# Performance work log

Hardware: AMD Instinct MI355X
Metric: run time of the kernel (lower is better)

Reference implementation:

```python
import jax, jax.numpy as jnp
import numpy as np
from jax import lax

G, NPER, K = 64, 1024, 512          # graphs, nodes per graph, kept per graph (ceil(0.5*1024))
N, E = G * NPER, 1_048_576          # total nodes, total edges
F, H, C = 128, 128, 10              # in_feats, hidden_dim, num_classes


def gcn(x, src, dst, ew, W, b, num_nodes):
    """PyG GCNConv: D^{-1/2}(A+I)D^{-1/2} X W + b, with edge weights ew."""
    xw = x @ W                                              # [N, H]
    deg = jax.ops.segment_sum(ew, dst, num_segments=num_nodes) + 1.0  # +1 self loop
    dinv = lax.rsqrt(deg)
    coef = dinv[src] * dinv[dst] * ew                       # [E]
    agg = jax.ops.segment_sum(coef[:, None] * xw[src], dst, num_segments=num_nodes)
    return agg + (dinv * dinv)[:, None] * xw + b            # self-loop term + bias


def setup_inputs() -> dict:
    key = jax.random.key(0)
    ks = jax.random.split(key, 10)
    x = jax.random.normal(ks[0], (N, F), jnp.float32)
    # intra-graph random edges: dst forced into same graph block as src
    src = jax.random.randint(ks[1], (E,), 0, N, dtype=jnp.int32)
    dst = (src // NPER) * NPER + jax.random.randint(ks[2], (E,), 0, NPER, dtype=jnp.int32)
    edge_index = jnp.stack([src, dst])                      # [2, E]
    batch = jnp.repeat(jnp.arange(G, dtype=jnp.int32), NPER)
    W1 = jax.random.normal(ks[3], (F, H), jnp.float32) / np.sqrt(F)
    b1 = jnp.zeros((H,), jnp.float32)
    p = jax.random.normal(ks[4], (H,), jnp.float32) / np.sqrt(H)   # TopKPooling score vector
    W2 = jax.random.normal(ks[5], (H, H), jnp.float32) / np.sqrt(H)
    b2 = jnp.zeros((H,), jnp.float32)
    Wl = jax.random.normal(ks[6], (H, C), jnp.float32) / np.sqrt(H)
    bl = jnp.zeros((C,), jnp.float32)
    return dict(x=x, edge_index=edge_index, batch=batch, W1=W1, b1=b1, p=p, W2=W2, b2=b2, Wl=Wl, bl=bl)


def reference(x, edge_index, batch, W1, b1, p, W2, b2, Wl, bl):
    src, dst = edge_index[0], edge_index[1]
    ew1 = jnp.ones((E,), x.dtype)
    h = jax.nn.relu(gcn(x, src, dst, ew1, W1, b1, N))       # conv1 + relu

    # --- TopKPooling: score = tanh(x.p/||p||), keep top-K per graph, gate x by score ---
    score = jnp.tanh((h @ p) / jnp.linalg.norm(p))          # [N]
    vals, idx = lax.top_k(score.reshape(G, NPER), K)        # per-graph top-k, [G, K]
    perm = (idx + jnp.arange(G, dtype=idx.dtype)[:, None] * NPER).reshape(-1)  # global ids [G*K]
    h2 = h[perm] * vals.reshape(-1, 1)                      # gated kept nodes [G*K, H]

    # edge re-index: keep only edges with both endpoints surviving (mask via weight 0)
    new_id = jnp.full((N,), -1, jnp.int32).at[perm].set(jnp.arange(G * K, dtype=jnp.int32))
    s2, d2 = new_id[src], new_id[dst]
    mask = (s2 >= 0) & (d2 >= 0)
    ew2 = mask.astype(h.dtype)
    s2 = jnp.where(mask, s2, 0)
    d2 = jnp.where(mask, d2, 0)

    h3 = jax.nn.relu(gcn(h2, s2, d2, ew2, W2, b2, G * K))   # conv2 + relu

    pooled = h3.reshape(G, K, H).mean(axis=1)               # global_mean_pool (equal counts)
    return pooled @ Wl + bl                                 # [G, C]
```

## Files before the change

kernel.cpp:

```cpp
#include <hip/hip_runtime.h>

#define NNODES 65536
#define NEDGES 1048576
#define NGRAPH 64
#define NPERG  1024
#define KEEP   512
#define M2     (NGRAPH * KEEP)
#define HD     128
#define NC     10
#define EMAX   20480

#define OW1 0
#define OW2 16384
#define OWL 32768
#define OB1 34048
#define OB2 34176
#define OP  34304
#define OBL 34432
#define NCVT 34448

typedef __attribute__((ext_vector_type(8))) short bf16x8;
typedef __attribute__((ext_vector_type(4))) float f32x4;

__device__ __forceinline__ float bf2f(unsigned short u) {
    return __uint_as_float(((unsigned int)u) << 16);
}
__device__ __forceinline__ unsigned short f2bf(float f) {
    unsigned int u = __float_as_uint(f);
    unsigned int r = (u + 0x7FFFu + ((u >> 16) & 1u)) >> 16;
    return (unsigned short)r;
}

__global__ __launch_bounds__(256) void prep_kernel(
    const void* __restrict__ W1, const void* __restrict__ b1, const void* __restrict__ p,
    const void* __restrict__ W2, const void* __restrict__ b2, const void* __restrict__ Wl,
    const void* __restrict__ bl, int* __restrict__ flag, float* __restrict__ cw,
    float* __restrict__ invnorm, int* __restrict__ new_id, int* __restrict__ ghist,
    int* __restrict__ gcur0, float* __restrict__ pooled,
    unsigned short* __restrict__ w1t, unsigned short* __restrict__ w2t) {
    int bid = blockIdx.x, t = threadIdx.x;
    const unsigned short* w1u = (const unsigned short*)W1;
    int local = 0;
    for (int i = t; i < 512; i += 256) {
        unsigned short u = w1u[2 * i];
        int e = (u >> 7) & 0xFF;
        local += (e >= 100 && e <= 140) ? 1 : 0;
    }
    __shared__ int red[256];
    red[t] = local;
    __syncthreads();
    for (int off = 128; off; off >>= 1) {
        if (t < off) red[t] += red[t + off];
        __syncthreads();
    }
    int fl = (red[0] >= 384) ? 1 : 0;
    if (bid == 0 && t == 0) flag[0] = fl;

    if (bid < 135) {
        int gid = bid * 256 + t;
        if (gid < NCVT) {
            const void* srcp; int idx;
            if (gid < OB1) {
                if (gid < OW2)      { srcp = W1; idx = gid - OW1; }
                else if (gid < OWL) { srcp = W2; idx = gid - OW2; }
                else                { srcp = Wl; idx = gid - OWL; }
            } else {
                if (gid < OB2)      { srcp = b1; idx = gid - OB1; }
                else if (gid < OP)  { srcp = b2; idx = gid - OB2; }
                else if (gid < OBL) { srcp = p;  idx = gid - OP; }
                else                { srcp = bl; idx = gid - OBL; }
            }
            float v;
            if (gid >= OWL && gid < OB1 && idx >= 1280) v = 0.f;
            else if (gid >= OBL && idx >= NC) v = 0.f;
            else if (fl) v = bf2f(((const unsigned short*)srcp)[idx]);
            else v = ((const float*)srcp)[idx];
            cw[gid] = v;
            if (gid < OW2) {
                int k = gid >> 7, n = gid & 127;
                w1t[n * 128 + k] = f2bf(v);
            } else if (gid < OWL) {
                int r = gid - OW2;
                int k = r >> 7, n = r & 127;
                w2t[n * 128 + k] = f2bf(v);
            }
        }
    } else if (bid == 135) {
        __shared__ float s2a[128];
        float pv = 0.f;
        if (t < 128) pv = fl ? bf2f(((const unsigned short*)p)[t]) : ((const float*)p)[t];
        if (t < 128) s2a[t] = pv * pv;
        __syncthreads();
        for (int off = 64; off; off >>= 1) {
            if (t < off) s2a[t] += s2a[t + off];
            __syncthreads();
        }
        if (t == 0) invnorm[0] = 1.0f / sqrtf(s2a[0]);
    } else {
        int i = (bid - 136) * 256 + t;
        new_id[i] = -1;
        if (i < NGRAPH) { ghist[i] = 0; gcur0[i] = 0; }
        if (i < NGRAPH * HD) pooled[i] = 0.f;
    }
}

__global__ __launch_bounds__(256) void hist_kernel(const int* __restrict__ src,
                                                   int* __restrict__ ghist) {
    __shared__ int lh[NGRAPH];
    int tid = threadIdx.x;
    if (tid < NGRAPH) lh[tid] = 0;
    __syncthreads();
    int e0 = blockIdx.x * 4096;
    for (int k = 0; k < 16; k++) atomicAdd(&lh[src[e0 + k * 256 + tid] >> 10], 1);
    __syncthreads();
    if (tid < NGRAPH) atomicAdd(&ghist[tid], lh[tid]);
}
__global__ __launch_bounds__(256) void binpass_kernel(const int* __restrict__ src,
                                                      const int* __restrict__ dst,
                                                      const int* __restrict__ ghist,
                                                      int* __restrict__ gcur0,
                                                      unsigned int* __restrict__ elist) {
    __shared__ int gh[NGRAPH];
    __shared__ int gbS[NGRAPH];
    __shared__ int lh[NGRAPH];
    __shared__ int lbase[NGRAPH];
    int tid = threadIdx.x;
    if (tid < NGRAPH) { gh[tid] = ghist[tid]; lh[tid] = 0; }
    __syncthreads();
    if (tid == 0) {
        int s = 0;
        for (int i = 0; i < NGRAPH; i++) { gbS[i] = s; s += gh[i]; }
    }
    __syncthreads();
    int e0 = blockIdx.x * 4096;
    int gs[16]; unsigned int pk[16];
    for (int k = 0; k < 16; k++) {
        int e = e0 + k * 256 + tid;
        int s = src[e], d = dst[e];
        gs[k] = s >> 10;
        pk[k] = (unsigned)(s & 1023) | ((unsigned)(d & 1023) << 10);
        atomicAdd(&lh[gs[k]], 1);
    }
    __syncthreads();
    if (tid < NGRAPH) { lbase[tid] = gbS[tid] + atomicAdd(&gcur0[tid], lh[tid]); lh[tid] = 0; }
    __syncthreads();
    for (int k = 0; k < 16; k++) {
        int g = gs[k];
        int pos = lbase[g] + atomicAdd(&lh[g], 1);
        elist[pos] = pk[k];
    }
}

__global__ __launch_bounds__(1024) void g1csr_kernel(
    const unsigned int* __restrict__ elist, const int* __restrict__ ghist,
    unsigned short* __restrict__ csr16, int* __restrict__ node_base,
    int* __restrict__ deg_out, float* __restrict__ dinv_out,
    const void* __restrict__ Araw, const unsigned short* __restrict__ Wtb,
    unsigned int* __restrict__ Cb, const int* __restrict__ flag) {
    __shared__ unsigned short sc[EMAX];
    __shared__ int cnt[NPERG];
    __shared__ int cur[NPERG];
    __shared__ int wsum[16];
    __shared__ int gh[NGRAPH];
    __shared__ int baseS, nS;
    int bid = blockIdx.x, t = threadIdx.x;
    if (bid < NGRAPH) {
        int g = bid;
        cnt[t] = 0;
        if (t < NGRAPH) gh[t] = ghist[t];
        __syncthreads();
        if (t == 0) {
            int s = 0;
            for (int i = 0; i < g; i++) s += gh[i];
            baseS = s; nS = gh[g];
        }
        __syncthreads();
        int base = baseS;
        int n = nS; if (n > EMAX) n = EMAX;
        for (int j = t; j < n; j += 1024) atomicAdd(&cnt[(elist[base + j] >> 10) & 1023], 1);
        __syncthreads();
        int v = cnt[t];
        int lane = t & 63;
        int x = v;
        for (int off = 1; off < 64; off <<= 1) {
            int y = __shfl_up(x, off);
            if (lane >= off) x += y;
        }
        if (lane == 63) wsum[t >> 6] = x;
        __syncthreads();
        if (t < 16) {
            int wv = wsum[t];
            int wx = wv;
            for (int off = 1; off < 16; off <<= 1) {
                int y = __shfl_up(wx, off);
                if (t >= off) wx += y;
            }
            wsum[t] = wx - wv;
        }
        __syncthreads();
        int excl = x - v + wsum[t >> 6];
        cur[t] = excl;
        deg_out[g * NPERG + t] = v;
        dinv_out[g * NPERG + t] = rsqrtf((float)v + 1.0f);
        node_base[g * NPERG + t] = base + excl;
        __syncthreads();
        for (int j = t; j < n; j += 1024) {
            unsigned int pk = elist[base + j];
            int d = (pk >> 10) & 1023;
            int pos = atomicAdd(&cur[d], 1);
            sc[pos] = (unsigned short)(pk & 1023);
        }
        __syncthreads();
        for (int j = t; j < n; j += 1024) csr16[base + j] = sc[j];
        return;
    }
    int row0 = (bid - NGRAPH) * 256;
    int wave = t >> 6, lane = t & 63;
    int r0 = row0 + wave * 16;
    int row = r0 + (lane & 15);
    int ko = (lane >> 4) * 8;
    f32x4 acc[8];
#pragma unroll
    for (int c = 0; c < 8; c++) acc[c] = (f32x4){0.f, 0.f, 0.f, 0.f};
    bf16x8 afr[4];
    if (flag[0]) {
        const unsigned short* arow = (const unsigned short*)Araw + (size_t)row * HD + ko;
#pragma unroll
        for (int kk = 0; kk < 4; kk++) afr[kk] = *(const bf16x8*)(arow + kk * 32);
    } else {
        const float* arow = (const float*)Araw + (size_t)row * HD + ko;
#pragma unroll
        for (int kk = 0; kk < 4; kk++) {
            float4 f0 = *(const float4*)(arow + kk * 32);
            float4 f1 = *(const float4*)(arow + kk * 32 + 4);
            bf16x8 a;
            a[0] = (short)f2bf(f0.x); a[1] = (short)f2bf(f0.y);
            a[2] = (short)f2bf(f0.z); a[3] = (short)f2bf(f0.w);
            a[4] = (short)f2bf(f1.x); a[5] = (short)f2bf(f1.y);
            a[6] = (short)f2bf(f1.z); a[7] = (short)f2bf(f1.w);
            afr[kk] = a;
        }
    }
    const unsigned short* brow = Wtb + (lane & 15) * HD + ko;
#pragma unroll
    for (int kk = 0; kk < 4; kk++) {
#pragma unroll
        for (int c = 0; c < 8; c++) {
            bf16x8 b = *(const bf16x8*)(brow + c * 16 * HD + kk * 32);
            acc[c] = __builtin_amdgcn_mfma_f32_16x16x32_bf16(afr[kk], b, acc[c], 0, 0, 0);
        }
    }
    int orow0 = r0 + (lane >> 4) * 4;
    bool even = !(lane & 1);
#pragma unroll
    for (int c = 0; c < 8; c++) {
#pragma unroll
        for (int j = 0; j < 4; j++) {
            float v = acc[c][j];
            float pt = __shfl_xor(v, 1);
            if (even) {
                unsigned int u = (unsigned int)f2bf(v) | ((unsigned int)f2bf(pt) << 16);
                Cb[(size_t)(orow0 + j) * 64 + ((c * 16 + (lane & 15)) >> 1)] = u;
            }
        }
    }
}

__global__ __launch_bounds__(256) void s1_pull(const unsigned short* __restrict__ csr16,
                                               const int* __restrict__ node_base,
                                               const int* __restrict__ deg,
                                               const float* __restrict__ dinv,
                                               const unsigned int* __restrict__ xwb,
                                               const float* __restrict__ b1,
                                               const float* __restrict__ pvec,
                                               const float* __restrict__ invnorm,
                                               float* __restrict__ h,
                                               float* __restrict__ score) {
    int b = blockIdx.x;
    int xcd = b & 7, j = b >> 3;
    int g = (j >> 8) * 8 + xcd;
    int n = g * NPERG + (j & 255) * 4 + (threadIdx.x >> 6);
    int lane = threadIdx.x & 63;
    int gb = g * NPERG;
    int base = node_base[n], cnt = deg[n];
    int e = 0; float ds = 0.f;
    if (lane < cnt) {
        e = csr16[base + lane];
        ds = dinv[gb + e];
    }
    float a0 = 0.f, a1 = 0.f;
    int klim = cnt < 64 ? cnt : 64;
    int k = 0;
    for (; k + 3 < klim; k += 4) {
        int s0 = __shfl(e, k), s1 = __shfl(e, k + 1);
        int s2 = __shfl(e, k + 2), s3 = __shfl(e, k + 3);
        float d0 = __shfl(ds, k), d1 = __shfl(ds, k + 1);
        float d2 = __shfl(ds, k + 2), d3 = __shfl(ds, k + 3);
        unsigned int u0 = xwb[(size_t)(gb + s0) * 64 + lane];
        unsigned int u1 = xwb[(size_t)(gb + s1) * 64 + lane];
        unsigned int u2 = xwb[(size_t)(gb + s2) * 64 + lane];
        unsigned int u3 = xwb[(size_t)(gb + s3) * 64 + lane];
        a0 += d0 * __uint_as_float(u0 << 16); a1 += d0 * __uint_as_float(u0 & 0xFFFF0000u);
        a0 += d1 * __uint_as_float(u1 << 16); a1 += d1 * __uint_as_float(u1 & 0xFFFF0000u);
        a0 += d2 * __uint_as_float(u2 << 16); a1 += d2 * __uint_as_float(u2 & 0xFFFF0000u);
        a0 += d3 * __uint_as_float(u3 << 16); a1 += d3 * __uint_as_float(u3 & 0xFFFF0000u);
    }
    for (; k < klim; k++) {
        int sk = __shfl(e, k);
        float dk = __shfl(ds, k);
        unsigned int u = xwb[(size_t)(gb + sk) * 64 + lane];
        a0 += dk * __uint_as_float(u << 16); a1 += dk * __uint_as_float(u & 0xFFFF0000u);
    }
    for (; k < cnt; k++) {
        int sk = csr16[base + k];
        float dk = dinv[gb + sk];
        unsigned int u = xwb[(size_t)(gb + sk) * 64 + lane];
        a0 += dk * __uint_as_float(u << 16); a1 += dk * __uint_as_float(u & 0xFFFF0000u);
    }
    float dn = dinv[n];
    float self = dn * dn;
    unsigned int us = xwb[(size_t)n * 64 + lane];
    float2 bb = ((const float2*)b1)[lane];
    float h0 = fmaxf(dn * a0 + self * __uint_as_float(us << 16) + bb.x, 0.f);
    float h1 = fmaxf(dn * a1 + self * __uint_as_float(us & 0xFFFF0000u) + bb.y, 0.f);
    float2 ho = {h0, h1};
    ((float2*)h)[(size_t)n * 64 + lane] = ho;
    float2 pp = ((const float2*)pvec)[lane];
    float sv = h0 * pp.x + h1 * pp.y;
    for (int off = 32; off; off >>= 1) sv += __shfl_down(sv, off);
    if (lane == 0) score[n] = tanhf(sv * invnorm[0]);
}

__global__ __launch_bounds__(1024) void topk_kernel(const float* __restrict__ score,
                                                    float* __restrict__ vals,
                                                    int* __restrict__ perm,
                                                    int* __restrict__ new_id) {
    __shared__ float sv[1024];
    __shared__ int si[1024];
    int g = blockIdx.x, t = threadIdx.x;
    sv[t] = score[g * NPERG + t];
    si[t] = t;
    __syncthreads();
    for (int k = 2; k <= 1024; k <<= 1) {
        for (int j = k >> 1; j > 0; j >>= 1) {
            int l = t ^ j;
            if (l > t) {
                bool desc = ((t & k) == 0);
                float va = sv[t], vb = sv[l];
                int ia = si[t], ib = si[l];
                bool gab = (va > vb) || (va == vb && ia < ib);
                if (gab != desc) { sv[t] = vb; si[t] = ib; sv[l] = va; si[l] = ia; }
            }
            __syncthreads();
        }
    }
    if (t < KEEP) {
        int node = g * NPERG + si[t];
        int slot = g * KEEP + t;
        vals[slot] = sv[t];
        perm[slot] = node;
        new_id[node] = slot;
    }
}

__global__ __launch_bounds__(512) void g2deg_kernel(
    const unsigned int* __restrict__ elist, const int* __restrict__ ghist,
    const int* __restrict__ new_id, float* __restrict__ dinv2,
    const float* __restrict__ h, const int* __restrict__ perm,
    const float* __restrict__ vals, const unsigned short* __restrict__ Wtb,
    float* __restrict__ C) {
    __shared__ int d2[KEEP];
    __shared__ int gh[NGRAPH];
    __shared__ int baseS, nS;
    int bid = blockIdx.x, t = threadIdx.x;
    if (bid < NGRAPH) {
        int g = bid;
        if (t < KEEP) d2[t] = 0;
        if (t < NGRAPH) gh[t] = ghist[t];
        __syncthreads();
        if (t == 0) {
            int s = 0;
            for (int i = 0; i < g; i++) s += gh[i];
            baseS = s; nS = gh[g];
        }
        __syncthreads();
        int base = baseS, n = nS;
        int gb = g * NPERG;
        int kb = g * KEEP;
        for (int j = t; j < n; j += 512) {
            unsigned int pk = elist[base + j];
            int s = pk & 1023, d = (pk >> 10) & 1023;
            int ns = new_id[gb + s], nd = new_id[gb + d];
            if (ns >= 0 && nd >= 0) atomicAdd(&d2[nd - kb], 1);
        }
        __syncthreads();
        if (t < KEEP) dinv2[kb + t] = rsqrtf((float)d2[t] + 1.0f);
        return;
    }
    int row0 = (bid - NGRAPH) * 128;
    int wave = t >> 6, lane = t & 63;
    int r0 = row0 + wave * 16;
    int m = r0 + (lane & 15);
    int ko = (lane >> 4) * 8;
    float sc = vals[m];
    const float* arow = h + (size_t)perm[m] * HD + ko;
    bf16x8 afr[4];
#pragma unroll
    for (int kk = 0; kk < 4; kk++) {
        float4 f0 = *(const float4*)(arow + kk * 32);
        float4 f1 = *(const float4*)(arow + kk * 32 + 4);
        bf16x8 a;
        a[0] = (short)f2bf(f0.x * sc); a[1] = (short)f2bf(f0.y * sc);
        a[2] = (short)f2bf(f0.z * sc); a[3] = (short)f2bf(f0.w * sc);
        a[4] = (short)f2bf(f1.x * sc); a[5] = (short)f2bf(f1.y * sc);
        a[6] = (short)f2bf(f1.z * sc); a[7] = (short)f2bf(f1.w * sc);
        afr[kk] = a;
    }
    f32x4 acc[8];
#pragma unroll
    for (int c = 0; c < 8; c++) acc[c] = (f32x4){0.f, 0.f, 0.f, 0.f};
    const unsigned short* brow = Wtb + (lane & 15) * HD + ko;
#pragma unroll
    for (int kk = 0; kk < 4; kk++) {
#pragma unroll
        for (int c = 0; c < 8; c++) {
            bf16x8 b = *(const bf16x8*)(brow + c * 16 * HD + kk * 32);
            acc[c] = __builtin_amdgcn_mfma_f32_16x16x32_bf16(afr[kk], b, acc[c], 0, 0, 0);
        }
    }
    int orow0 = r0 + (lane >> 4) * 4;
    bool even = !(lane & 1);
    float2* C2 = (float2*)C;
#pragma unroll
    for (int c = 0; c < 8; c++) {
#pragma unroll
        for (int j = 0; j < 4; j++) {
            float v = acc[c][j];
            float pt = __shfl_xor(v, 1);
            if (even) {
                float2 o = {v, pt};
                C2[(size_t)(orow0 + j) * 64 + ((c * 16 + (lane & 15)) >> 1)] = o;
            }
        }
    }
}

__global__ __launch_bounds__(256) void s2_pull(const unsigned short* __restrict__ csr16,
                                               const int* __restrict__ node_base,
                                               const int* __restrict__ deg,
                                               const int* __restrict__ perm,
                                               const int* __restrict__ new_id,
                                               const float* __restrict__ dinv2,
                                               const float* __restrict__ xw2,
                                               const float* __restrict__ b2,
                                               float* __restrict__ pooled) {
    __shared__ float pr[HD];
    __shared__ int cnk[4][64];
    __shared__ float cds[4][64];
    int tid = threadIdx.x;
    if (tid < HD) pr[tid] = 0.f;
    __syncthreads();
    int b = blockIdx.x;
    int xcd = b & 7, j = b >> 3;
    int g = (j >> 7) * 8 + xcd;
    int wv = tid >> 6;
    int m = g * KEEP + (j & 127) * 4 + wv;
    int lane = tid & 63;
    int node = perm[m];
    int gb = node & ~(NPERG - 1);
    int base = node_base[node], cnt = deg[node];
    int nk = 0; float ds = 0.f;
    if (lane < cnt) {
        int ns = new_id[gb + csr16[base + lane]];
        if (ns >= 0) { nk = ns; ds = dinv2[ns]; }
    }
    unsigned long long msk = __ballot(ds != 0.f);
    int pos = __popcll(msk & ((1ull << lane) - 1ull));
    if (ds != 0.f) { cnk[wv][pos] = nk; cds[wv][pos] = ds; }
    int na = __popcll(msk);
    const float2* xf2 = (const float2*)xw2;
    float a0 = 0.f, a1 = 0.f;
    int k = 0;
    for (; k + 3 < na; k += 4) {
        int s0 = cnk[wv][k], s1 = cnk[wv][k + 1];
        int s2 = cnk[wv][k + 2], s3 = cnk[wv][k + 3];
        float d0 = cds[wv][k], d1 = cds[wv][k + 1];
        float d2 = cds[wv][k + 2], d3 = cds[wv][k + 3];
        float2 v0 = xf2[(size_t)s0 * 64 + lane];
        float2 v1 = xf2[(size_t)s1 * 64 + lane];
        float2 v2 = xf2[(size_t)s2 * 64 + lane];
        float2 v3 = xf2[(size_t)s3 * 64 + lane];
        a0 += d0 * v0.x; a1 += d0 * v0.y;
        a0 += d1 * v1.x; a1 += d1 * v1.y;
        a0 += d2 * v2.x; a1 += d2 * v2.y;
        a0 += d3 * v3.x; a1 += d3 * v3.y;
    }
    for (; k < na; k++) {
        int sk = cnk[wv][k];
        float dk = cds[wv][k];
        float2 v = xf2[(size_t)sk * 64 + lane];
        a0 += dk * v.x; a1 += dk * v.y;
    }
    for (int kk = 64; kk < cnt; kk++) {
        int ns = new_id[gb + csr16[base + kk]];
        if (ns >= 0) {
            float dk = dinv2[ns];
            float2 v = xf2[(size_t)ns * 64 + lane];
            a0 += dk * v.x; a1 += dk * v.y;
        }
    }
    float dn = dinv2[m];
    float self = dn * dn;
    float2 xs = xf2[(size_t)m * 64 + lane];
    float2 bb = ((const float2*)b2)[lane];
    float o0 = fmaxf(dn * a0 + self * xs.x + bb.x, 0.f);
    float o1 = fmaxf(dn * a1 + self * xs.y + bb.y, 0.f);
    atomicAdd(&pr[lane * 2], o0);
    atomicAdd(&pr[lane * 2 + 1], o1);
    __syncthreads();
    if (tid < HD) atomicAdd(&pooled[g * HD + tid], pr[tid]);
}

__global__ __launch_bounds__(128) void outk_kernel(const float* __restrict__ pooled,
                                                   const float* __restrict__ Wl,
                                                   const float* __restrict__ bl,
                                                   void* __restrict__ outv,
                                                   const int* __restrict__ flag) {
    int g = blockIdx.x, t = threadIdx.x;
    __shared__ float sp[HD];
    sp[t] = pooled[g * HD + t] * (1.0f / KEEP);
    __syncthreads();
    if (t < NC) {
        float acc = bl[t];
        for (int hh = 0; hh < HD; hh++) acc += sp[hh] * Wl[hh * NC + t];
        if (flag[0]) ((unsigned short*)outv)[g * NC + t] = f2bf(acc);
        else         ((float*)outv)[g * NC + t] = acc;
    }
}

extern "C" void kernel_launch(void* const* d_in, const int* in_sizes, int n_in,
                              void* d_out, int out_size, void* d_ws, size_t ws_size,
                              hipStream_t stream) {
    const int* ei   = (const int*)d_in[1];
    const int* srcv = ei;
    const int* dstv = ei + NEDGES;

    char* w = (char*)d_ws;
    const size_t MB = 1u << 20;
    const size_t KB = 1024;
    float* dinv1     = (float*)(w + 0);
    float* score     = (float*)(w + 256 * KB);
    float* vals      = (float*)(w + 512 * KB);
    int*   perm      = (int*)(w + 640 * KB);
    int*   new_id    = (int*)(w + 768 * KB);
    int*   deg1      = (int*)(w + 1024 * KB);
    int*   node_base = (int*)(w + 1280 * KB);
    float* dinv2     = (float*)(w + 1536 * KB);
    float* invnorm   = (float*)(w + 1664 * KB);
    int*   flag      = (int*)(w + 1664 * KB + 64);
    int*   ghist     = (int*)(w + 1664 * KB + 1024);
    int*   gcur0     = (int*)(w + 1664 * KB + 2048);
    float* cw        = (float*)(w + 1700 * KB);
    float* pooled    = (float*)(w + 1840 * KB);
    unsigned short* w1t = (unsigned short*)(w + 1880 * KB);
    unsigned short* w2t = (unsigned short*)(w + 1912 * KB);
    unsigned int* xw1b = (unsigned int*)(w + 2 * MB);
    float* xw2  = (float*)(w + 18 * MB);
    float* agg  = (float*)(w + 34 * MB);
    unsigned int* elist    = (unsigned int*)(w + 66 * MB);
    unsigned short* csr16  = (unsigned short*)(w + 70 * MB);

    float* W1f = cw + OW1; float* W2f = cw + OW2; float* Wlf = cw + OWL;
    float* b1f = cw + OB1; float* b2f = cw + OB2; float* pf  = cw + OP;
    float* blf = cw + OBL;
    (void)W1f; (void)W2f;

    prep_kernel<<<392, 256, 0, stream>>>(d_in[3], d_in[4], d_in[5], d_in[6], d_in[7],
                                         d_in[8], d_in[9], flag, cw, invnorm, new_id,
                                         ghist, gcur0, pooled, w1t, w2t);
    hist_kernel<<<256, 256, 0, stream>>>(srcv, ghist);
    binpass_kernel<<<256, 256, 0, stream>>>(srcv, dstv, ghist, gcur0, elist);
    g1csr_kernel<<<NGRAPH + NNODES / 256, 1024, 0, stream>>>(
        elist, ghist, csr16, node_base, deg1, dinv1, d_in[0], w1t, xw1b, flag);
    s1_pull<<<NNODES / 4, 256, 0, stream>>>(csr16, node_base, deg1, dinv1, xw1b, b1f, pf,
                                            invnorm, agg, score);
    topk_kernel<<<NGRAPH, 1024, 0, stream>>>(score, vals, perm, new_id);
    g2deg_kernel<<<NGRAPH + M2 / 128, 512, 0, stream>>>(
        elist, ghist, new_id, dinv2, agg, perm, vals, w2t, xw2);
    s2_pull<<<M2 / 4, 256, 0, stream>>>(csr16, node_base, deg1, perm, new_id, dinv2,
                                        xw2, b2f, pooled);
    outk_kernel<<<NGRAPH, 128, 0, stream>>>(pooled, Wlf, blf, d_out, flag);

    (void)in_sizes; (void)n_in; (void)out_size; (void)ws_size;
}
```

Before: 264.7 us.

## Fuse edge histogram into prep, store conv1 output as bf16, unroll gather by eight

Moves the per-graph source-edge histogram into extra blocks of the prep kernel, which now write per-block partial histograms. The binning kernel reduces those partials itself, so one launch and the global atomics are gone. The conv1 output h is stored as packed bf16 instead of fp32, halving the write in s1_pull and the gathered read in g2deg. The s1_pull neighbour gather gains an 8-wide unrolled loop to keep more loads in flight. The cost is an extra rounding of h before the gating multiply, and every binpass block redundantly re-reducing 256×64 partials.

```diff
diff --git a/kernel.cpp b/kernel.cpp
--- a/kernel.cpp
+++ b/kernel.cpp
@@ -37,7 +37,8 @@
     const void* __restrict__ bl, int* __restrict__ flag, float* __restrict__ cw,
     float* __restrict__ invnorm, int* __restrict__ new_id, int* __restrict__ ghist,
     int* __restrict__ gcur0, float* __restrict__ pooled,
-    unsigned short* __restrict__ w1t, unsigned short* __restrict__ w2t) {
+    unsigned short* __restrict__ w1t, unsigned short* __restrict__ w2t,
+    const int* __restrict__ src, int* __restrict__ phist) {
     int bid = blockIdx.x, t = threadIdx.x;
     const unsigned short* w1u = (const unsigned short*)W1;
     int local = 0;
@@ -47,6 +48,7 @@
         local += (e >= 100 && e <= 140) ? 1 : 0;
     }
     __shared__ int red[256];
+    __shared__ int lh[NGRAPH];
     red[t] = local;
     __syncthreads();
     for (int off = 128; off; off >>= 1) {
@@ -96,36 +98,45 @@
             __syncthreads();
         }
         if (t == 0) invnorm[0] = 1.0f / sqrtf(s2a[0]);
-    } else {
+    } else if (bid < 392) {
         int i = (bid - 136) * 256 + t;
         new_id[i] = -1;
         if (i < NGRAPH) { ghist[i] = 0; gcur0[i] = 0; }
         if (i < NGRAPH * HD) pooled[i] = 0.f;
-    }
-}
-
-__global__ __launch_bounds__(256) void hist_kernel(const int* __restrict__ src,
-                                                   int* __restrict__ ghist) {
-    __shared__ int lh[NGRAPH];
-    int tid = threadIdx.x;
-    if (tid < NGRAPH) lh[tid] = 0;
-    __syncthreads();
-    int e0 = blockIdx.x * 4096;
-    for (int k = 0; k < 16; k++) atomicAdd(&lh[src[e0 + k * 256 + tid] >> 10], 1);
-    __syncthreads();
-    if (tid < NGRAPH) atomicAdd(&ghist[tid], lh[tid]);
-}
+    } else {
+        if (t < NGRAPH) lh[t] = 0;
+        __syncthreads();
+        int e0 = (bid - 392) * 4096;
+        for (int k = 0; k < 16; k++) atomicAdd(&lh[src[e0 + k * 256 + t] >> 10], 1);
+        __syncthreads();
+        if (t < NGRAPH) phist[(bid - 392) * 64 + t] = lh[t];
+    }
+}
+
 __global__ __launch_bounds__(256) void binpass_kernel(const int* __restrict__ src,
                                                       const int* __restrict__ dst,
-                                                      const int* __restrict__ ghist,
+                                                      const int* __restrict__ phist,
+                                                      int* __restrict__ ghist,
                                                       int* __restrict__ gcur0,
                                                       unsigned int* __restrict__ elist) {
     __shared__ int gh[NGRAPH];
     __shared__ int gbS[NGRAPH];
     __shared__ int lh[NGRAPH];
     __shared__ int lbase[NGRAPH];
+    __shared__ int qsum[4][NGRAPH];
     int tid = threadIdx.x;
-    if (tid < NGRAPH) { gh[tid] = ghist[tid]; lh[tid] = 0; }
+    {
+        int g = tid & 63, q = tid >> 6;
+        int s = 0;
+        for (int b = q * 64; b < q * 64 + 64; b++) s += phist[b * 64 + g];
+        qsum[q][g] = s;
+    }
+    __syncthreads();
+    if (tid < NGRAPH) {
+        gh[tid] = qsum[0][tid] + qsum[1][tid] + qsum[2][tid] + qsum[3][tid];
+        lh[tid] = 0;
+        if (blockIdx.x == 0) ghist[tid] = gh[tid];
+    }
     __syncthreads();
     if (tid == 0) {
         int s = 0;
@@ -274,7 +285,7 @@
                                                const float* __restrict__ b1,
                                                const float* __restrict__ pvec,
                                                const float* __restrict__ invnorm,
-                                               float* __restrict__ h,
+                                               unsigned int* __restrict__ hb,
                                                float* __restrict__ score) {
     int b = blockIdx.x;
     int xcd = b & 7, j = b >> 3;
@@ -291,6 +302,32 @@
     float a0 = 0.f, a1 = 0.f;
     int klim = cnt < 64 ? cnt : 64;
     int k = 0;
+    for (; k + 7 < klim; k += 8) {
+        int s0 = __shfl(e, k),     s1 = __shfl(e, k + 1);
+        int s2 = __shfl(e, k + 2), s3 = __shfl(e, k + 3);
+        int s4 = __shfl(e, k + 4), s5 = __shfl(e, k + 5);
+        int s6 = __shfl(e, k + 6), s7 = __shfl(e, k + 7);
+        float d0 = __shfl(ds, k),     d1 = __shfl(ds, k + 1);
+        float d2 = __shfl(ds, k + 2), d3 = __shfl(ds, k + 3);
+        float d4 = __shfl(ds, k + 4), d5 = __shfl(ds, k + 5);
+        float d6 = __shfl(ds, k + 6), d7 = __shfl(ds, k + 7);
+        unsigned int u0 = xwb[(size_t)(gb + s0) * 64 + lane];
+        unsigned int u1 = xwb[(size_t)(gb + s1) * 64 + lane];
+        unsigned int u2 = xwb[(size_t)(gb + s2) * 64 + lane];
+        unsigned int u3 = xwb[(size_t)(gb + s3) * 64 + lane];
+        unsigned int u4 = xwb[(size_t)(gb + s4) * 64 + lane];
+        unsigned int u5 = xwb[(size_t)(gb + s5) * 64 + lane];
+        unsigned int u6 = xwb[(size_t)(gb + s6) * 64 + lane];
+        unsigned int u7 = xwb[(size_t)(gb + s7) * 64 + lane];
+        a0 += d0 * __uint_as_float(u0 << 16); a1 += d0 * __uint_as_float(u0 & 0xFFFF0000u);
+        a0 += d1 * __uint_as_float(u1 << 16); a1 += d1 * __uint_as_float(u1 & 0xFFFF0000u);
+        a0 += d2 * __uint_as_float(u2 << 16); a1 += d2 * __uint_as_float(u2 & 0xFFFF0000u);
+        a0 += d3 * __uint_as_float(u3 << 16); a1 += d3 * __uint_as_float(u3 & 0xFFFF0000u);
+        a0 += d4 * __uint_as_float(u4 << 16); a1 += d4 * __uint_as_float(u4 & 0xFFFF0000u);
+        a0 += d5 * __uint_as_float(u5 << 16); a1 += d5 * __uint_as_float(u5 & 0xFFFF0000u);
+        a0 += d6 * __uint_as_float(u6 << 16); a1 += d6 * __uint_as_float(u6 & 0xFFFF0000u);
+        a0 += d7 * __uint_as_float(u7 << 16); a1 += d7 * __uint_as_float(u7 & 0xFFFF0000u);
+    }
     for (; k + 3 < klim; k += 4) {
         int s0 = __shfl(e, k), s1 = __shfl(e, k + 1);
         int s2 = __shfl(e, k + 2), s3 = __shfl(e, k + 3);
@@ -323,8 +360,7 @@
     float2 bb = ((const float2*)b1)[lane];
     float h0 = fmaxf(dn * a0 + self * __uint_as_float(us << 16) + bb.x, 0.f);
     float h1 = fmaxf(dn * a1 + self * __uint_as_float(us & 0xFFFF0000u) + bb.y, 0.f);
-    float2 ho = {h0, h1};
-    ((float2*)h)[(size_t)n * 64 + lane] = ho;
+    hb[(size_t)n * 64 + lane] = (unsigned int)f2bf(h0) | ((unsigned int)f2bf(h1) << 16);
     float2 pp = ((const float2*)pvec)[lane];
     float sv = h0 * pp.x + h1 * pp.y;
     for (int off = 32; off; off >>= 1) sv += __shfl_down(sv, off);
@@ -366,7 +402,7 @@
 __global__ __launch_bounds__(512) void g2deg_kernel(
     const unsigned int* __restrict__ elist, const int* __restrict__ ghist,
     const int* __restrict__ new_id, float* __restrict__ dinv2,
-    const float* __restrict__ h, const int* __restrict__ perm,
+    const unsigned int* __restrict__ hb, const int* __restrict__ perm,
     const float* __restrict__ vals, const unsigned short* __restrict__ Wtb,
     float* __restrict__ C) {
     __shared__ int d2[KEEP];
@@ -403,17 +439,20 @@
     int m = r0 + (lane & 15);
     int ko = (lane >> 4) * 8;
     float sc = vals[m];
-    const float* arow = h + (size_t)perm[m] * HD + ko;
+    const unsigned int* arow = hb + (size_t)perm[m] * 64 + (ko >> 1);
     bf16x8 afr[4];
 #pragma unroll
     for (int kk = 0; kk < 4; kk++) {
-        float4 f0 = *(const float4*)(arow + kk * 32);
-        float4 f1 = *(const float4*)(arow + kk * 32 + 4);
+        uint4 q = *(const uint4*)(arow + kk * 16);
         bf16x8 a;
-        a[0] = (short)f2bf(f0.x * sc); a[1] = (short)f2bf(f0.y * sc);
-        a[2] = (short)f2bf(f0.z * sc); a[3] = (short)f2bf(f0.w * sc);
-        a[4] = (short)f2bf(f1.x * sc); a[5] = (short)f2bf(f1.y * sc);
-        a[6] = (short)f2bf(f1.z * sc); a[7] = (short)f2bf(f1.w * sc);
+        a[0] = (short)f2bf(bf2f((unsigned short)q.x) * sc);
+        a[1] = (short)f2bf(bf2f((unsigned short)(q.x >> 16)) * sc);
+        a[2] = (short)f2bf(bf2f((unsigned short)q.y) * sc);
+        a[3] = (short)f2bf(bf2f((unsigned short)(q.y >> 16)) * sc);
+        a[4] = (short)f2bf(bf2f((unsigned short)q.z) * sc);
+        a[5] = (short)f2bf(bf2f((unsigned short)(q.z >> 16)) * sc);
+        a[6] = (short)f2bf(bf2f((unsigned short)q.w) * sc);
+        a[7] = (short)f2bf(bf2f((unsigned short)(q.w >> 16)) * sc);
         afr[kk] = a;
     }
     f32x4 acc[8];
@@ -564,9 +603,10 @@
     float* pooled    = (float*)(w + 1840 * KB);
     unsigned short* w1t = (unsigned short*)(w + 1880 * KB);
     unsigned short* w2t = (unsigned short*)(w + 1912 * KB);
+    int* phist       = (int*)(w + 1944 * KB);
     unsigned int* xw1b = (unsigned int*)(w + 2 * MB);
     float* xw2  = (float*)(w + 18 * MB);
-    float* agg  = (float*)(w + 34 * MB);
+    unsigned int* hb = (unsigned int*)(w + 34 * MB);
     unsigned int* elist    = (unsigned int*)(w + 66 * MB);
     unsigned short* csr16  = (unsigned short*)(w + 70 * MB);
 
@@ -575,18 +615,17 @@
     float* blf = cw + OBL;
     (void)W1f; (void)W2f;
 
-    prep_kernel<<<392, 256, 0, stream>>>(d_in[3], d_in[4], d_in[5], d_in[6], d_in[7],
+    prep_kernel<<<648, 256, 0, stream>>>(d_in[3], d_in[4], d_in[5], d_in[6], d_in[7],
                                          d_in[8], d_in[9], flag, cw, invnorm, new_id,
-                                         ghist, gcur0, pooled, w1t, w2t);
-    hist_kernel<<<256, 256, 0, stream>>>(srcv, ghist);
-    binpass_kernel<<<256, 256, 0, stream>>>(srcv, dstv, ghist, gcur0, elist);
+                                         ghist, gcur0, pooled, w1t, w2t, srcv, phist);
+    binpass_kernel<<<256, 256, 0, stream>>>(srcv, dstv, phist, ghist, gcur0, elist);
     g1csr_kernel<<<NGRAPH + NNODES / 256, 1024, 0, stream>>>(
         elist, ghist, csr16, node_base, deg1, dinv1, d_in[0], w1t, xw1b, flag);
     s1_pull<<<NNODES / 4, 256, 0, stream>>>(csr16, node_base, deg1, dinv1, xw1b, b1f, pf,
-                                            invnorm, agg, score);
+                                            invnorm, hb, score);
     topk_kernel<<<NGRAPH, 1024, 0, stream>>>(score, vals, perm, new_id);
     g2deg_kernel<<<NGRAPH + M2 / 128, 512, 0, stream>>>(
-        elist, ghist, new_id, dinv2, agg, perm, vals, w2t, xw2);
+        elist, ghist, new_id, dinv2, hb, perm, vals, w2t, xw2);
     s2_pull<<<M2 / 4, 256, 0, stream>>>(csr16, node_base, deg1, perm, new_id, dinv2,
                                         xw2, b2f, pooled);
     outk_kernel<<<NGRAPH, 128, 0, stream>>>(pooled, Wlf, blf, d_out, flag);
```

New measurement: 261.9 us. About the same (-1.1%).
